# Kernel tuning notes

Hardware: AMD Instinct MI355X
Metric: run time of the kernel (lower is better)

Reference implementation:

```python
import jax, jax.numpy as jnp
import numpy as np

A = 312          # nb_attributes
LAT = 64         # latent_dim per attribute
HID = 128        # hidden_dim per attribute
OUT = 1          # output_dim per attribute
B = 8192         # batch


def setup_inputs() -> dict:
    key = jax.random.key(0)
    k1, k2, k3, k4, k5 = jax.random.split(key, 5)
    x = jax.random.normal(k1, (B, A * LAT), dtype=jnp.float32)
    # block-diagonal weights: one small matrix per attribute
    W1 = jax.random.normal(k2, (A, LAT, HID), dtype=jnp.float32) * (1.0 / np.sqrt(LAT))
    b1 = jax.random.normal(k3, (A, HID), dtype=jnp.float32) * 0.01
    W2 = jax.random.normal(k4, (A, HID, OUT), dtype=jnp.float32) * (1.0 / np.sqrt(HID))
    b2 = jax.random.normal(k5, (A, OUT), dtype=jnp.float32) * 0.01
    return {"x": x, "W1": W1, "b1": b1, "W2": W2, "b2": b2}


def reference(x, W1, b1, W2, b2):
    # BlockLinear 1: [B, A*LAT] -> view [B, A, LAT] -> per-attribute matmul -> [B, A, HID]
    xb = x.reshape(B, A, LAT)
    h = jnp.einsum('bal,alh->bah', xb, W1) + b1[None]   # [B, A, HID]
    h = jax.nn.relu(h)
    # BlockLinear 2: [B, A, HID] -> [B, A, OUT]
    o = jnp.einsum('bah,aho->bao', h, W2) + b2[None]    # [B, A, OUT]
    o = jax.nn.sigmoid(o)
    return o.reshape(B, A * OUT)
```

## Files before the change

### kernel.cpp

```cpp
#include <hip/hip_runtime.h>

#define NA   312
#define LAT  64
#define HID  128
#define NB   8192
#define MB   128
#define NBT  (NB / MB)

typedef __attribute__((ext_vector_type(8))) short bf16x8;
typedef __attribute__((ext_vector_type(4))) float f32x4;

__device__ inline short f2bf(float f) {
    unsigned u = __builtin_bit_cast(unsigned, f);
    u += 0x7FFFu + ((u >> 16) & 1u);
    return (short)(u >> 16);
}

__global__ __launch_bounds__(256, 4) void attr_decoder_mfma(
    const float* __restrict__ x,
    const float* __restrict__ W1,
    const float* __restrict__ b1,
    const float* __restrict__ W2,
    const float* __restrict__ b2,
    float* __restrict__ out)
{
    __shared__ short w1T[HID * LAT];
    __shared__ float b1s[HID];
    __shared__ float w2s[HID];
    __shared__ float b2s_;

    const int tid = threadIdx.x;
    const int a   = blockIdx.x >> 6;
    const int bt  = blockIdx.x & (NBT - 1);

    {
        const float4* wg = reinterpret_cast<const float4*>(W1 + (size_t)a * (LAT * HID));
        char* w1b = reinterpret_cast<char*>(w1T);
        #pragma unroll
        for (int i = 0; i < (LAT * HID / 4) / 256; ++i) {
            const int flat4 = i * 256 + tid;
            float4 v = wg[flat4];
            const int flat = flat4 * 4;
            const int k  = flat >> 7;
            const int n0 = flat & 127;
            float vv[4] = {v.x, v.y, v.z, v.w};
            #pragma unroll
            for (int j = 0; j < 4; ++j) {
                const int n = n0 + j;
                const int byteaddr = (n * 128 + k * 2) ^ ((n & 7) << 4);
                *reinterpret_cast<short*>(w1b + byteaddr) = f2bf(vv[j]);
            }
        }
        if (tid < HID) {
            b1s[tid] = b1[a * HID + tid];
            w2s[tid] = W2[a * HID + tid];
        }
        if (tid == 0) b2s_ = b2[a];
    }
    __syncthreads();

    const int w    = tid >> 6;
    const int lane = tid & 63;
    const int llo  = lane & 15;
    const int lhi  = lane >> 4;
    const int rowbase = bt * MB + w * 32;

    bf16x8 afrag[2][2];
    #pragma unroll
    for (int mt = 0; mt < 2; ++mt) {
        const float* xrow = x + (size_t)(rowbase + mt * 16 + llo) * (NA * LAT)
                              + (size_t)a * LAT;
        #pragma unroll
        for (int kk = 0; kk < 2; ++kk) {
            const float4* p = reinterpret_cast<const float4*>(xrow + kk * 32 + lhi * 8);
            float4 v0 = p[0];
            float4 v1 = p[1];
            bf16x8 f;
            f[0] = f2bf(v0.x); f[1] = f2bf(v0.y); f[2] = f2bf(v0.z); f[3] = f2bf(v0.w);
            f[4] = f2bf(v1.x); f[5] = f2bf(v1.y); f[6] = f2bf(v1.z); f[7] = f2bf(v1.w);
            afrag[mt][kk] = f;
        }
    }

    const char* w1b = reinterpret_cast<const char*>(w1T);
    float p2[2][4] = {};
    #pragma unroll
    for (int nt = 0; nt < 8; ++nt) {
        const int n = nt * 16 + llo;
        bf16x8 bfrag[2];
        #pragma unroll
        for (int kk = 0; kk < 2; ++kk) {
            const int byteaddr = (n * 128 + (kk * 32 + lhi * 8) * 2) ^ ((n & 7) << 4);
            bfrag[kk] = *reinterpret_cast<const bf16x8*>(w1b + byteaddr);
        }
        const float w2v = w2s[n];
        const float b1v = b1s[n];
        #pragma unroll
        for (int mt = 0; mt < 2; ++mt) {
            f32x4 acc = {0.f, 0.f, 0.f, 0.f};
            acc = __builtin_amdgcn_mfma_f32_16x16x32_bf16(afrag[mt][0], bfrag[0], acc, 0, 0, 0);
            acc = __builtin_amdgcn_mfma_f32_16x16x32_bf16(afrag[mt][1], bfrag[1], acc, 0, 0, 0);
            #pragma unroll
            for (int r = 0; r < 4; ++r) {
                const float h = fmaxf(acc[r] + b1v, 0.f);
                p2[mt][r] = fmaf(h, w2v, p2[mt][r]);
            }
        }
    }

    const float ob = b2s_;
    #pragma unroll
    for (int mt = 0; mt < 2; ++mt) {
        #pragma unroll
        for (int r = 0; r < 4; ++r) {
            float s = p2[mt][r];
            s += __shfl_xor(s, 1);
            s += __shfl_xor(s, 2);
            s += __shfl_xor(s, 4);
            s += __shfl_xor(s, 8);
            s = 1.0f / (1.0f + expf(-(s + ob)));
            if (llo == 0) {
                const int row = rowbase + mt * 16 + lhi * 4 + r;
                out[(size_t)row * NA + a] = s;
            }
        }
    }
}

extern "C" void kernel_launch(void* const* d_in, const int* in_sizes, int n_in,
                              void* d_out, int out_size, void* d_ws, size_t ws_size,
                              hipStream_t stream) {
    const float* x  = (const float*)d_in[0];
    const float* W1 = (const float*)d_in[1];
    const float* b1 = (const float*)d_in[2];
    const float* W2 = (const float*)d_in[3];
    const float* b2 = (const float*)d_in[4];
    float* out = (float*)d_out;

    dim3 grid(NA * NBT);
    dim3 block(256);
    hipLaunchKernelGGL(attr_decoder_mfma, grid, block, 0, stream,
                       x, W1, b1, W2, b2, out);
}
```

Before: 209.9 us.

## Pre-pack W1 into MFMA fragment layout in a separate kernel, double rows per block

A new prep kernel converts each attribute's W1 to bf16 once and stores it in global workspace already laid out as MFMA B-fragments. This removes the per-block LDS staging, conversion and barrier from the main kernel. The main kernel now reads fragments directly from global/L2, handles 256 rows per block (four M-tiles per wave), and folds b1 into the accumulator's initial value. The trade-off is an extra launch, more registers per wave, and half as many blocks.

```diff
diff --git a/kernel.cpp b/kernel.cpp
--- a/kernel.cpp
+++ b/kernel.cpp
@@ -4,8 +4,9 @@
 #define LAT  64
 #define HID  128
 #define NB   8192
-#define MB   128
+#define MB   256
 #define NBT  (NB / MB)
+#define MT   4
 
 typedef __attribute__((ext_vector_type(8))) short bf16x8;
 typedef __attribute__((ext_vector_type(4))) float f32x4;
@@ -16,58 +17,57 @@
     return (short)(u >> 16);
 }
 
-__global__ __launch_bounds__(256, 4) void attr_decoder_mfma(
+__global__ __launch_bounds__(256, 2) void prep_w1(
+    const float* __restrict__ W1, short* __restrict__ w1f)
+{
+    __shared__ float lds[LAT * HID];
+    const int a   = blockIdx.x;
+    const int tid = threadIdx.x;
+
+    const float4* src = reinterpret_cast<const float4*>(W1 + (size_t)a * (LAT * HID));
+    float4* ldsv = reinterpret_cast<float4*>(lds);
+    #pragma unroll
+    for (int i = 0; i < (LAT * HID / 4) / 256; ++i)
+        ldsv[i * 256 + tid] = src[i * 256 + tid];
+    __syncthreads();
+
+    bf16x8* dst = reinterpret_cast<bf16x8*>(w1f + (size_t)a * (LAT * HID));
+    #pragma unroll
+    for (int i = 0; i < 4; ++i) {
+        const int e    = i * 256 + tid;
+        const int nt   = e >> 7;
+        const int kk   = (e >> 6) & 1;
+        const int lane = e & 63;
+        const int n  = nt * 16 + (lane & 15);
+        const int k0 = kk * 32 + (lane >> 4) * 8;
+        bf16x8 f;
+        #pragma unroll
+        for (int j = 0; j < 8; ++j)
+            f[j] = f2bf(lds[(k0 + j) * HID + n]);
+        dst[e] = f;
+    }
+}
+
+__global__ __launch_bounds__(256, 4) void attr_decoder_main(
     const float* __restrict__ x,
-    const float* __restrict__ W1,
+    const short* __restrict__ w1f,
     const float* __restrict__ b1,
     const float* __restrict__ W2,
     const float* __restrict__ b2,
     float* __restrict__ out)
 {
-    __shared__ short w1T[HID * LAT];
-    __shared__ float b1s[HID];
-    __shared__ float w2s[HID];
-    __shared__ float b2s_;
-
-    const int tid = threadIdx.x;
-    const int a   = blockIdx.x >> 6;
-    const int bt  = blockIdx.x & (NBT - 1);
-
-    {
-        const float4* wg = reinterpret_cast<const float4*>(W1 + (size_t)a * (LAT * HID));
-        char* w1b = reinterpret_cast<char*>(w1T);
-        #pragma unroll
-        for (int i = 0; i < (LAT * HID / 4) / 256; ++i) {
-            const int flat4 = i * 256 + tid;
-            float4 v = wg[flat4];
-            const int flat = flat4 * 4;
-            const int k  = flat >> 7;
-            const int n0 = flat & 127;
-            float vv[4] = {v.x, v.y, v.z, v.w};
-            #pragma unroll
-            for (int j = 0; j < 4; ++j) {
-                const int n = n0 + j;
-                const int byteaddr = (n * 128 + k * 2) ^ ((n & 7) << 4);
-                *reinterpret_cast<short*>(w1b + byteaddr) = f2bf(vv[j]);
-            }
-        }
-        if (tid < HID) {
-            b1s[tid] = b1[a * HID + tid];
-            w2s[tid] = W2[a * HID + tid];
-        }
-        if (tid == 0) b2s_ = b2[a];
-    }
-    __syncthreads();
-
+    const int tid  = threadIdx.x;
+    const int a    = blockIdx.x >> 5;
+    const int bt   = blockIdx.x & (NBT - 1);
     const int w    = tid >> 6;
     const int lane = tid & 63;
     const int llo  = lane & 15;
     const int lhi  = lane >> 4;
-    const int rowbase = bt * MB + w * 32;
+    const int rowbase = bt * MB + w * 64;
 
-    bf16x8 afrag[2][2];
+    bf16x8 afrag[MT][2];
     #pragma unroll
-    for (int mt = 0; mt < 2; ++mt) {
+    for (int mt = 0; mt < MT; ++mt) {
         const float* xrow = x + (size_t)(rowbase + mt * 16 + llo) * (NA * LAT)
                               + (size_t)a * LAT;
         #pragma unroll
@@ -82,35 +82,32 @@
         }
     }
 
-    const char* w1b = reinterpret_cast<const char*>(w1T);
-    float p2[2][4] = {};
-    #pragma unroll
+    const bf16x8* wf = reinterpret_cast<const bf16x8*>(w1f + (size_t)a * (LAT * HID));
+    const float*  b1a = b1 + a * HID;
+    const float*  w2a = W2 + a * HID;
+    float p2[MT][4] = {};
+    #pragma unroll 2
     for (int nt = 0; nt < 8; ++nt) {
+        const bf16x8 bf0 = wf[(nt * 2 + 0) * 64 + lane];
+        const bf16x8 bf1 = wf[(nt * 2 + 1) * 64 + lane];
         const int n = nt * 16 + llo;
-        bf16x8 bfrag[2];
+        const float b1v = b1a[n];
+        const float w2v = w2a[n];
+        const f32x4 cin = {b1v, b1v, b1v, b1v};
         #pragma unroll
-        for (int kk = 0; kk < 2; ++kk) {
-            const int byteaddr = (n * 128 + (kk * 32 + lhi * 8) * 2) ^ ((n & 7) << 4);
-            bfrag[kk] = *reinterpret_cast<const bf16x8*>(w1b + byteaddr);
-        }
-        const float w2v = w2s[n];
-        const float b1v = b1s[n];
-        #pragma unroll
-        for (int mt = 0; mt < 2; ++mt) {
-            f32x4 acc = {0.f, 0.f, 0.f, 0.f};
-            acc = __builtin_amdgcn_mfma_f32_16x16x32_bf16(afrag[mt][0], bfrag[0], acc, 0, 0, 0);
-            acc = __builtin_amdgcn_mfma_f32_16x16x32_bf16(afrag[mt][1], bfrag[1], acc, 0, 0, 0);
+        for (int mt = 0; mt < MT; ++mt) {
+            f32x4 acc = cin;
+            acc = __builtin_amdgcn_mfma_f32_16x16x32_bf16(afrag[mt][0], bf0, acc, 0, 0, 0);
+            acc = __builtin_amdgcn_mfma_f32_16x16x32_bf16(afrag[mt][1], bf1, acc, 0, 0, 0);
             #pragma unroll
-            for (int r = 0; r < 4; ++r) {
-                const float h = fmaxf(acc[r] + b1v, 0.f);
-                p2[mt][r] = fmaf(h, w2v, p2[mt][r]);
-            }
+            for (int r = 0; r < 4; ++r)
+                p2[mt][r] = fmaf(fmaxf(acc[r], 0.f), w2v, p2[mt][r]);
         }
     }
 
-    const float ob = b2s_;
+    const float ob = b2[a];
     #pragma unroll
-    for (int mt = 0; mt < 2; ++mt) {
+    for (int mt = 0; mt < MT; ++mt) {
         #pragma unroll
         for (int r = 0; r < 4; ++r) {
             float s = p2[mt][r];
@@ -136,9 +133,9 @@
     const float* W2 = (const float*)d_in[3];
     const float* b2 = (const float*)d_in[4];
     float* out = (float*)d_out;
+    short* w1f = (short*)d_ws;
 
-    dim3 grid(NA * NBT);
-    dim3 block(256);
-    hipLaunchKernelGGL(attr_decoder_mfma, grid, block, 0, stream,
-                       x, W1, b1, W2, b2, out);
+    hipLaunchKernelGGL(prep_w1, dim3(NA), dim3(256), 0, stream, W1, w1f);
+    hipLaunchKernelGGL(attr_decoder_main, dim3(NA * NBT), dim3(256), 0, stream,
+                       x, w1f, b1, W2, b2, out);
 }
```

After: 178.1 us. 15.1% less time.
